# Performance work log

Hardware: AMD Instinct MI355X
Metric: run time of the kernel (lower is better)

Reference implementation:

```python
import jax, jax.numpy as jnp
import numpy as np

NUM_GRAPHS = 2048  # number of graphs in the batch (max batch id + 1)


def setup_inputs() -> dict:
    key = jax.random.key(0)
    ks = jax.random.split(key, 8)
    N, E, ND, ED, H = 100000, 400000, 256, 128, 128
    IN = ND * 3 + ED  # 896
    h = jax.random.normal(ks[0], (N, ND), dtype=jnp.float32)
    ei = jax.random.randint(ks[1], (2, E), 0, N, dtype=jnp.int64)
    ea = jax.random.normal(ks[2], (E, ED), dtype=jnp.float32)
    batch = jnp.sort(jax.random.randint(ks[3], (N,), 0, NUM_GRAPHS, dtype=jnp.int64))
    W1 = jax.random.normal(ks[4], (IN, H), dtype=jnp.float32) * (1.0 / np.sqrt(IN))
    b1 = jnp.zeros((H,), dtype=jnp.float32)
    W2 = jax.random.normal(ks[5], (H, 1), dtype=jnp.float32) * (1.0 / np.sqrt(H))
    b2 = jnp.zeros((1,), dtype=jnp.float32)
    return {"h": h, "ei": ei, "ea": ea, "batch": batch,
            "W1": W1, "b1": b1, "W2": W2, "b2": b2}


def reference(h, ei, ea, batch, W1, b1, W2, b2):
    s, t = ei[0], ei[1]
    # global_mean_pool: per-graph mean of node features
    sums = jax.ops.segment_sum(h, batch, num_segments=NUM_GRAPHS)          # [B, ND]
    counts = jax.ops.segment_sum(jnp.ones((h.shape[0],), h.dtype), batch,
                                 num_segments=NUM_GRAPHS)                   # [B]
    pooled = sums / jnp.maximum(counts, 1.0)[:, None]
    g = pooled[batch[s]]                                                    # [E, ND]
    x = jnp.concatenate([h[s], h[t], ea, g], axis=-1)                       # [E, 3*ND+ED]
    hid = jnp.maximum(x @ W1 + b1, 0.0)
    return hid @ W2 + b2                                                    # [E, 1]
```

## Files before the change

### kernel.cpp

```cpp
#include <hip/hip_runtime.h>
#include <hip/hip_bf16.h>


typedef __attribute__((ext_vector_type(8))) short bf16x8;
typedef __attribute__((ext_vector_type(4))) float f32x4;
typedef __attribute__((address_space(3))) char lds_char;
typedef __attribute__((address_space(1))) const void g_cvoid;

constexpr int kND = 256;
constexpr int kED = 128;
constexpr int kH  = 128;
constexpr int kB  = 2048;
constexpr int TM  = 128;
constexpr int kNF = 224;

__device__ __forceinline__ void gl2lds16(const void* gsrc, lds_char* ldst) {
  __builtin_amdgcn_global_load_lds((g_cvoid*)gsrc,
                                   (__attribute__((address_space(3))) void*)ldst,
                                   16, 0, 0);
}

__device__ __forceinline__ ushort f2bf(float x) {
  union { float f; unsigned u; } c; c.f = x;
  unsigned u = c.u + 0x7FFFu + ((c.u >> 16) & 1u);
  return (ushort)(u >> 16);
}
__device__ __forceinline__ float bf2f(ushort x) {
  union { unsigned u; float f; } c; c.u = ((unsigned)x) << 16;
  return c.f;
}
__device__ __forceinline__ bool data_is_f32(const void* p) {
  const unsigned* u = (const unsigned*)p;
  int cnt = 0;
  #pragma unroll
  for (int i = 0; i < 64; ++i) {
    unsigned e = (u[i] >> 7) & 0xFFu;
    cnt += (e >= 90u && e <= 140u) ? 1 : 0;
  }
  return cnt < 40;
}
__device__ __forceinline__ bool idx_is_64(const int* __restrict__ p) {
  return ((p[1] | p[3] | p[5] | p[7]) == 0) && ((p[0] | p[2] | p[4] | p[6]) != 0);
}
__device__ __forceinline__ float loadf(const void* p, int i, bool isf32) {
  return isf32 ? ((const float*)p)[i] : bf2f(((const ushort*)p)[i]);
}

__global__ __launch_bounds__(256) void pool_kernel(
    const void* __restrict__ hv, ushort* __restrict__ hbf, int preconv,
    const int* __restrict__ batch, const int* __restrict__ ei, int N,
    ushort* __restrict__ pooled) {
  const bool isf32 = data_is_f32(hv);
  const bool is64 = idx_is_64(ei);
  const int b = blockIdx.x, tid = threadIdx.x;
  __shared__ int bounds[2];
  __shared__ float sred[8][kND];
  if (tid < 2) {
    int target = b + tid;
    int lo = 0, hi = N;
    while (lo < hi) {
      int mid = (lo + hi) >> 1;
      int v = is64 ? batch[2 * mid] : batch[mid];
      if (v < target) lo = mid + 1; else hi = mid;
    }
    bounds[tid] = lo;
  }
  __syncthreads();
  const int lo = bounds[0], hi = bounds[1];
  const int dg = tid & 31;
  const int rstr = tid >> 5;
  float a[8];
  #pragma unroll
  for (int j = 0; j < 8; ++j) a[j] = 0.f;

  if (!isf32) {
    const ushort* base = (const ushort*)hv + dg * 8;
    int r = lo + rstr;
    for (; r + 8 < hi; r += 16) {
      union { uint4 v; ushort us[8]; } u0, u1;
      u0.v = *(const uint4*)(base + (size_t)r * kND);
      u1.v = *(const uint4*)(base + (size_t)(r + 8) * kND);
      #pragma unroll
      for (int j = 0; j < 8; ++j) a[j] += bf2f(u0.us[j]);
      #pragma unroll
      for (int j = 0; j < 8; ++j) a[j] += bf2f(u1.us[j]);
    }
    for (; r < hi; r += 8) {
      union { uint4 v; ushort us[8]; } u0;
      u0.v = *(const uint4*)(base + (size_t)r * kND);
      #pragma unroll
      for (int j = 0; j < 8; ++j) a[j] += bf2f(u0.us[j]);
    }
  } else if (preconv) {
    const float* base = (const float*)hv + dg * 8;
    ushort* wb = hbf + dg * 8;
    for (int r = lo + rstr; r < hi; r += 8) {
      float4 f0 = *(const float4*)(base + (size_t)r * kND);
      float4 f1 = *(const float4*)(base + (size_t)r * kND + 4);
      union { ushort us[8]; uint4 v; } cv;
      cv.us[0] = f2bf(f0.x); cv.us[1] = f2bf(f0.y);
      cv.us[2] = f2bf(f0.z); cv.us[3] = f2bf(f0.w);
      cv.us[4] = f2bf(f1.x); cv.us[5] = f2bf(f1.y);
      cv.us[6] = f2bf(f1.z); cv.us[7] = f2bf(f1.w);
      *(uint4*)(wb + (size_t)r * kND) = cv.v;
      a[0] += f0.x; a[1] += f0.y; a[2] += f0.z; a[3] += f0.w;
      a[4] += f1.x; a[5] += f1.y; a[6] += f1.z; a[7] += f1.w;
    }
  } else {
    const float* base = (const float*)hv + dg * 8;
    for (int r = lo + rstr; r < hi; r += 8) {
      float4 f0 = *(const float4*)(base + (size_t)r * kND);
      float4 f1 = *(const float4*)(base + (size_t)r * kND + 4);
      a[0] += f0.x; a[1] += f0.y; a[2] += f0.z; a[3] += f0.w;
      a[4] += f1.x; a[5] += f1.y; a[6] += f1.z; a[7] += f1.w;
    }
  }
  #pragma unroll
  for (int j = 0; j < 8; ++j) sred[rstr][dg * 8 + j] = a[j];
  __syncthreads();
  int cnt = hi - lo; if (cnt < 1) cnt = 1;
  float inv = 1.f / (float)cnt;
  float s = 0.f;
  #pragma unroll
  for (int st = 0; st < 8; ++st) s += sred[st][tid];
  pooled[(size_t)b * kND + tid] = f2bf(s * inv);
}

__global__ __launch_bounds__(256) void build_wfrag(
    const void* __restrict__ W1v, ushort* __restrict__ Wfrag) {
  const bool isf32 = data_is_f32(W1v);
  int idx = blockIdx.x * 256 + threadIdx.x;
  if (idx >= kNF * 64) return;
  int l = idx & 63, f = idx >> 6;
  int ni = f & 3, nhi = (f >> 2) & 1, ksg = f >> 3;
  int tile = ksg >> 2;
  int basek = (tile == 0) ? 512 : ((tile < 5) ? (tile - 1) * 128 : tile * 128);
  int n = nhi * 64 + ni * 16 + (l & 15);
  int k0 = basek + (ksg & 3) * 32 + (l >> 4) * 8;
  union { ushort us[8]; uint4 v; } cv;
  #pragma unroll
  for (int j = 0; j < 8; ++j)
    cv.us[j] = f2bf(loadf(W1v, (k0 + j) * kH + n, isf32));
  *(uint4*)(Wfrag + (size_t)f * 512 + l * 8) = cv.v;
}

template<bool HB, bool EA32> struct TD;
template<> struct TD<true, true> {
  static constexpr int NT = 8;
  static constexpr int ty[8]  = {0,0,1,1,2,2,3,3};
  static constexpr int sub[8] = {0,1,0,1,0,1,0,1};
  static constexpr int ksc[8] = {2,2,4,4,4,4,4,4};
  static constexpr int kg0[8] = {0,2,4,8,12,16,20,24};
  static constexpr bool tf32[8] = {1,1,0,0,0,0,0,0};
};
template<> struct TD<true, false> {
  static constexpr int NT = 7;
  static constexpr int ty[7]  = {0,1,1,2,2,3,3};
  static constexpr int sub[7] = {0,0,1,0,1,0,1};
  static constexpr int ksc[7] = {4,4,4,4,4,4,4};
  static constexpr int kg0[7] = {0,4,8,12,16,20,24};
  static constexpr bool tf32[7] = {0,0,0,0,0,0,0};
};
template<> struct TD<false, true> {
  static constexpr int NT = 12;
  static constexpr int ty[12]  = {0,0,1,1,1,1,2,2,2,2,3,3};
  static constexpr int sub[12] = {0,1,0,1,2,3,0,1,2,3,0,1};
  static constexpr int ksc[12] = {2,2,2,2,2,2,2,2,2,2,4,4};
  static constexpr int kg0[12] = {0,2,4,6,8,10,12,14,16,18,20,24};
  static constexpr bool tf32[12] = {1,1,1,1,1,1,1,1,1,1,0,0};
};
template<> struct TD<false, false> {
  static constexpr int NT = 11;
  static constexpr int ty[11]  = {0,1,1,1,1,2,2,2,2,3,3};
  static constexpr int sub[11] = {0,0,1,2,3,0,1,2,3,0,1};
  static constexpr int ksc[11] = {4,2,2,2,2,2,2,2,2,4,4};
  static constexpr int kg0[11] = {0,4,6,8,10,12,14,16,18,20,24};
  static constexpr bool tf32[11] = {0,1,1,1,1,1,1,1,1,0,0};
};

template<bool HB, bool EA32>
__device__ __forceinline__ void edge_core(
    const char* __restrict__ hsrc, const char* __restrict__ easrc,
    const ushort* __restrict__ pooled, const ushort* __restrict__ Wfrag,
    const char* XlB, lds_char* Xl3, const int* rs, const int* rt, const int* rg,
    int e0, int E, int wave, int lane, f32x4 (&acc)[4][2]) {
  using T = TD<HB, EA32>;
  const int l15 = lane & 15, quad = lane >> 4;
  const int mh = (wave & 1) * 64;
  const int nq = wave >> 1;
  const int nhi = nq >> 1;
  const int nlo = (nq & 1) * 2;
  const ushort* wl = Wfrag + (size_t)nhi * 2048 + lane * 8;
  const int cx0 = (lane & 15) * 16;
  const int rlane = lane >> 4;

  auto src_addr = [&](int t, int row) -> const char* {
    int cx = cx0 ^ ((row & 7) << 4);
    int ty = T::ty[t], sub = T::sub[t];
    if (ty == 0) {
      int e = e0 + row; if (e >= E) e = E - 1;
      return easrc + (size_t)e * (EA32 ? 512 : 256) + sub * 256 + cx;
    }
    if (ty == 1) return hsrc + (size_t)rs[row] * (HB ? 512 : 1024) + sub * 256 + cx;
    if (ty == 2) return hsrc + (size_t)rt[row] * (HB ? 512 : 1024) + sub * 256 + cx;
    return (const char*)pooled + (size_t)rg[row] * 512 + sub * 256 + cx;
  };
  auto stage = [&](int t) {
    lds_char* dst = Xl3 + (t & 1) * 32768;
    #pragma unroll
    for (int i = 0; i < 4; ++i) {
      int row = wave * 16 + i * 4 + rlane;
      gl2lds16(src_addr(t, row), dst + (wave * 16 + i * 4) * 256);
    }
  };

  stage(0);
  __syncthreads();

  #pragma unroll
  for (int t = 0; t < T::NT; ++t) {
    bf16x8 bq[8];
    #pragma unroll
    for (int ks = 0; ks < T::ksc[t]; ++ks)
      #pragma unroll
      for (int ni = 0; ni < 2; ++ni)
        bq[ks * 2 + ni] =
            *(const bf16x8*)(wl + (size_t)(T::kg0[t] + ks) * 4096 + (nlo + ni) * 512);
    __builtin_amdgcn_sched_barrier(0);
    if (t + 1 < T::NT) stage(t + 1);

    const char* xb = XlB + (t & 1) * 32768;
    #pragma unroll
    for (int ks = 0; ks < T::ksc[t]; ++ks) {
      bf16x8 af[4];
      #pragma unroll
      for (int mi = 0; mi < 4; ++mi) {
        int row = mh + mi * 16 + l15;
        int sz = (row & 7) << 4;
        const char* rb = xb + row * 256;
        if (T::tf32[t]) {
          int cb = ks * 128 + quad * 32;
          float4 f0 = *(const float4*)(rb + (cb ^ sz));
          float4 f1 = *(const float4*)(rb + ((cb + 16) ^ sz));
          union { ushort us[8]; bf16x8 v; } cv;
          cv.us[0] = f2bf(f0.x); cv.us[1] = f2bf(f0.y);
          cv.us[2] = f2bf(f0.z); cv.us[3] = f2bf(f0.w);
          cv.us[4] = f2bf(f1.x); cv.us[5] = f2bf(f1.y);
          cv.us[6] = f2bf(f1.z); cv.us[7] = f2bf(f1.w);
          af[mi] = cv.v;
        } else {
          int cb = ks * 64 + quad * 16;
          af[mi] = *(const bf16x8*)(rb + (cb ^ sz));
        }
      }
      #pragma unroll
      for (int mi = 0; mi < 4; ++mi)
        #pragma unroll
        for (int ni = 0; ni < 2; ++ni)
          acc[mi][ni] = __builtin_amdgcn_mfma_f32_16x16x32_bf16(
              af[mi], bq[ks * 2 + ni], acc[mi][ni], 0, 0, 0);
    }
    __syncthreads();
  }
}

__global__ __launch_bounds__(512, 4) void edge_kernel(
    const void* __restrict__ hv, const ushort* __restrict__ hbf, int preconv,
    const int* __restrict__ ei, const void* __restrict__ eav,
    const int* __restrict__ batch, const ushort* __restrict__ pooled,
    const ushort* __restrict__ Wfrag, const void* __restrict__ b1v,
    const void* __restrict__ W2v, const void* __restrict__ b2v,
    void* __restrict__ outv, int E) {
  __shared__ __align__(16) char XlB[2 * 32768];
  __shared__ int rs[TM], rt[TM], rg[TM];
  __shared__ float outacc[TM];
  __shared__ float b1s[kH], w2s[kH];
  lds_char* Xl3 = (lds_char*)XlB;

  const int tid = threadIdx.x;
  const int e0 = blockIdx.x * TM;
  const bool isf32 = data_is_f32(hv);
  const bool is64 = idx_is_64(ei);

  if (tid < TM) {
    int e = e0 + tid; if (e >= E) e = E - 1;
    int s = is64 ? ei[2 * e] : ei[e];
    int t = is64 ? ei[2 * (E + e)] : ei[E + e];
    rs[tid] = s;
    rt[tid] = t;
    rg[tid] = is64 ? batch[2 * s] : batch[s];
    w2s[tid] = loadf(W2v, tid, isf32);
    b1s[tid] = loadf(b1v, tid, isf32);
    outacc[tid] = 0.f;
  }
  __syncthreads();

  const int wave = tid >> 6, lane = tid & 63;
  const int l15 = lane & 15, quad = lane >> 4;
  const int mh = (wave & 1) * 64;
  const int nq = wave >> 1;
  const int nhi = nq >> 1;
  const int nlo = (nq & 1) * 2;

  f32x4 acc[4][2];
  #pragma unroll
  for (int i = 0; i < 4; ++i)
    #pragma unroll
    for (int j = 0; j < 2; ++j)
      acc[i][j] = (f32x4){0.f, 0.f, 0.f, 0.f};

  const bool hb = !isf32 || preconv;
  const char* hsrc = !isf32 ? (const char*)hv
                            : (preconv ? (const char*)hbf : (const char*)hv);
  const bool ea32 = data_is_f32(eav);

  if (hb) {
    if (ea32) edge_core<true, true >((const char*)hsrc, (const char*)eav, pooled,
                                     Wfrag, XlB, Xl3, rs, rt, rg, e0, E, wave, lane, acc);
    else      edge_core<true, false>((const char*)hsrc, (const char*)eav, pooled,
                                     Wfrag, XlB, Xl3, rs, rt, rg, e0, E, wave, lane, acc);
  } else {
    if (ea32) edge_core<false, true >((const char*)hsrc, (const char*)eav, pooled,
                                      Wfrag, XlB, Xl3, rs, rt, rg, e0, E, wave, lane, acc);
    else      edge_core<false, false>((const char*)hsrc, (const char*)eav, pooled,
                                      Wfrag, XlB, Xl3, rs, rt, rg, e0, E, wave, lane, acc);
  }

  float w2v[2], b1r[2];
  #pragma unroll
  for (int ni = 0; ni < 2; ++ni) {
    int n = nhi * 64 + (nlo + ni) * 16 + l15;
    w2v[ni] = w2s[n];
    b1r[ni] = b1s[n];
  }
  #pragma unroll
  for (int mi = 0; mi < 4; ++mi) {
    float ps[4] = {0.f, 0.f, 0.f, 0.f};
    #pragma unroll
    for (int ni = 0; ni < 2; ++ni)
      #pragma unroll
      for (int j = 0; j < 4; ++j) {
        float v = acc[mi][ni][j] + b1r[ni];
        ps[j] += (v > 0.f ? v : 0.f) * w2v[ni];
      }
    #pragma unroll
    for (int off = 1; off < 16; off <<= 1)
      #pragma unroll
      for (int j = 0; j < 4; ++j)
        ps[j] += __shfl_xor(ps[j], off, 64);
    if (l15 == 0)
      #pragma unroll
      for (int j = 0; j < 4; ++j)
        atomicAdd(&outacc[mh + mi * 16 + quad * 4 + j], ps[j]);
  }
  __syncthreads();
  if (tid < TM) {
    int e = e0 + tid;
    if (e < E) {
      float a = outacc[tid] + loadf(b2v, 0, isf32);
      if (isf32) ((float*)outv)[e] = a;
      else       ((ushort*)outv)[e] = f2bf(a);
    }
  }
}

extern "C" void kernel_launch(void* const* d_in, const int* in_sizes, int n_in,
                              void* d_out, int out_size, void* d_ws, size_t ws_size,
                              hipStream_t stream) {
  const void* h   = d_in[0];
  const int*  ei  = (const int*)d_in[1];
  const void* ea  = d_in[2];
  const int*  bat = (const int*)d_in[3];
  const void* W1  = d_in[4];
  const void* b1  = d_in[5];
  const void* W2  = d_in[6];
  const void* b2  = d_in[7];

  const int N = in_sizes[3];
  const int E = in_sizes[1] / 2;

  ushort* pooled = (ushort*)d_ws;
  ushort* Wfrag  = pooled + (size_t)kB * kND;
  ushort* hbf    = Wfrag + (size_t)kNF * 512;
  const size_t need =
      ((size_t)kB * kND + (size_t)kNF * 512 + (size_t)N * kND) * sizeof(ushort);
  const int preconv = (ws_size >= need) ? 1 : 0;

  pool_kernel<<<kB, 256, 0, stream>>>(h, hbf, preconv, bat, ei, N, pooled);
  build_wfrag<<<(kNF * 64 + 255) / 256, 256, 0, stream>>>(W1, Wfrag);
  edge_kernel<<<(E + TM - 1) / TM, 512, 0, stream>>>(
      h, hbf, preconv, ei, ea, bat, pooled, Wfrag, b1, W2, b2, d_out, E);
}
```

Baseline: 497.6 us.

## Precompute per-node and per-graph W1 projections, shrink edge GEMM to edge features

Splits the first layer by linearity. h@W1 slices are computed once per node, and pooled@W1 plus the bias once per graph; both are folded into a per-node fp32 table P12. The edge kernel then only runs an MFMA GEMM over the 128 edge-attribute columns and gathers two 128-float rows from P12 per edge before ReLU and the W2 dot. This removes the redundant per-edge GEMM over 768 gathered node and graph features, at the cost of a ~100 MB fp32 intermediate, extra launches, and scattered fp32 gathers in the edge epilogue.

```diff
diff --git a/kernel.cpp b/kernel.cpp
--- a/kernel.cpp
+++ b/kernel.cpp
@@ -124,6 +124,263 @@
   #pragma unroll
   for (int st = 0; st < 8; ++st) s += sred[st][tid];
   pooled[(size_t)b * kND + tid] = f2bf(s * inv);
+}
+
+__global__ __launch_bounds__(256) void pg_kernel(
+    const ushort* __restrict__ pooled, const void* __restrict__ W1v,
+    const void* __restrict__ b1v, float* __restrict__ Pg) {
+  const bool w32 = data_is_f32(W1v);
+  const bool b32 = data_is_f32(b1v);
+  const int tid = threadIdx.x;
+  const int g = blockIdx.x * 2 + (tid >> 7);
+  const int n = tid & 127;
+  float acc = loadf(b1v, n, b32);
+  const ushort* pr = pooled + (size_t)g * kND;
+  #pragma unroll 8
+  for (int k = 0; k < 256; ++k)
+    acc += bf2f(pr[k]) * loadf(W1v, (640 + k) * kH + n, w32);
+  Pg[(size_t)g * 128 + n] = acc;
+}
+
+__global__ __launch_bounds__(256) void build_wfrag2(
+    const void* __restrict__ W1v, ushort* __restrict__ WfragN) {
+  const bool isf32 = data_is_f32(W1v);
+  int idx = blockIdx.x * 256 + threadIdx.x;
+  if (idx >= 160 * 64) return;
+  int l = idx & 63, f = idx >> 6;
+  int row0, col;
+  int kj = (l >> 4) * 8;
+  if (f < 128) {
+    int ni = f & 3, nq = (f >> 2) & 3, ksg = f >> 4;
+    int n_l = nq * 64 + ni * 16 + (l & 15);
+    int k0 = ksg * 32 + kj;
+    row0 = (n_l < 128) ? k0 : (256 + k0);
+    col = n_l & 127;
+  } else {
+    int fe = f - 128;
+    int ni = fe & 3, nhi = (fe >> 2) & 1, ksg = fe >> 3;
+    int n = nhi * 64 + ni * 16 + (l & 15);
+    row0 = 512 + ksg * 32 + kj;
+    col = n;
+  }
+  union { ushort us[8]; uint4 v; } cv;
+  #pragma unroll
+  for (int j = 0; j < 8; ++j)
+    cv.us[j] = f2bf(loadf(W1v, (row0 + j) * kH + col, isf32));
+  *(uint4*)(WfragN + (size_t)f * 512 + l * 8) = cv.v;
+}
+
+__global__ __launch_bounds__(512, 4) void node_kernel(
+    const void* __restrict__ hv, const int* __restrict__ batch,
+    const int* __restrict__ ei, int N, const ushort* __restrict__ WfragN,
+    const float* __restrict__ Pg, float* __restrict__ P12) {
+  __shared__ __align__(16) char Xh[128 * 256];
+  __shared__ int gs[128];
+  const bool hf32 = data_is_f32(hv);
+  const bool is64 = idx_is_64(ei);
+  const int tid = threadIdx.x;
+  const int v0 = blockIdx.x * 128;
+
+  if (tid < 128) {
+    int v = v0 + tid; if (v >= N) v = N - 1;
+    gs[tid] = is64 ? batch[2 * v] : batch[v];
+  }
+
+  const int wave = tid >> 6, lane = tid & 63;
+  const int l15 = lane & 15, quad = lane >> 4;
+  const int mh = (wave & 1) * 64;
+  const int cq = wave >> 1;
+  const ushort* wl = WfragN + lane * 8;
+  const int r = tid >> 2, q = tid & 3;
+  int vr = v0 + r; if (vr >= N) vr = N - 1;
+
+  f32x4 acc[4][4];
+  #pragma unroll
+  for (int i = 0; i < 4; ++i)
+    #pragma unroll
+    for (int j = 0; j < 4; ++j)
+      acc[i][j] = (f32x4){0.f, 0.f, 0.f, 0.f};
+
+  for (int p = 0; p < 2; ++p) {
+    if (hf32) {
+      const float4* src = (const float4*)hv + (size_t)vr * 64 + p * 32 + q * 8;
+      #pragma unroll
+      for (int j = 0; j < 4; ++j) {
+        float4 f0 = src[2 * j], f1 = src[2 * j + 1];
+        union { ushort us[8]; uint4 v; } cv;
+        cv.us[0] = f2bf(f0.x); cv.us[1] = f2bf(f0.y);
+        cv.us[2] = f2bf(f0.z); cv.us[3] = f2bf(f0.w);
+        cv.us[4] = f2bf(f1.x); cv.us[5] = f2bf(f1.y);
+        cv.us[6] = f2bf(f1.z); cv.us[7] = f2bf(f1.w);
+        *(uint4*)&Xh[r * 256 + ((q * 64 + j * 16) ^ ((r & 7) << 4))] = cv.v;
+      }
+    } else {
+      const uint4* src = (const uint4*)hv + (size_t)vr * 32 + p * 16 + q * 4;
+      #pragma unroll
+      for (int j = 0; j < 4; ++j)
+        *(uint4*)&Xh[r * 256 + ((q * 64 + j * 16) ^ ((r & 7) << 4))] = src[j];
+    }
+    __syncthreads();
+    #pragma unroll
+    for (int ks = 0; ks < 4; ++ks) {
+      bf16x8 bq[4];
+      #pragma unroll
+      for (int ni = 0; ni < 4; ++ni)
+        bq[ni] = *(const bf16x8*)(wl +
+            (size_t)(((p * 4 + ks) * 16 + cq * 4 + ni)) * 512);
+      bf16x8 af[4];
+      #pragma unroll
+      for (int mi = 0; mi < 4; ++mi) {
+        int row = mh + mi * 16 + l15;
+        int cb = ks * 64 + quad * 16;
+        af[mi] = *(const bf16x8*)&Xh[row * 256 + (cb ^ ((row & 7) << 4))];
+      }
+      #pragma unroll
+      for (int mi = 0; mi < 4; ++mi)
+        #pragma unroll
+        for (int ni = 0; ni < 4; ++ni)
+          acc[mi][ni] = __builtin_amdgcn_mfma_f32_16x16x32_bf16(
+              af[mi], bq[ni], acc[mi][ni], 0, 0, 0);
+    }
+    __syncthreads();
+  }
+
+  #pragma unroll
+  for (int mi = 0; mi < 4; ++mi)
+    #pragma unroll
+    for (int ni = 0; ni < 4; ++ni) {
+      int col = cq * 64 + ni * 16 + l15;
+      #pragma unroll
+      for (int j = 0; j < 4; ++j) {
+        int row = mh + mi * 16 + quad * 4 + j;
+        int v = v0 + row;
+        if (v < N) {
+          float val = acc[mi][ni][j];
+          if (col < 128) val += Pg[(size_t)gs[row] * 128 + col];
+          P12[(size_t)v * 256 + col] = val;
+        }
+      }
+    }
+}
+
+__global__ __launch_bounds__(512, 4) void edge_kernel_new(
+    const void* __restrict__ hv, const int* __restrict__ ei,
+    const void* __restrict__ eav, const ushort* __restrict__ WfragE,
+    const float* __restrict__ P12, const void* __restrict__ W2v,
+    const void* __restrict__ b2v, void* __restrict__ outv, int E) {
+  __shared__ __align__(16) char Xe[128 * 256];
+  __shared__ int rs[TM], rt[TM];
+  __shared__ float outacc[TM];
+  __shared__ float w2s[kH];
+  const bool isf32 = data_is_f32(hv);
+  const bool ea32 = data_is_f32(eav);
+  const bool w232 = data_is_f32(W2v);
+  const bool is64 = idx_is_64(ei);
+  const int tid = threadIdx.x;
+  const int e0 = blockIdx.x * TM;
+
+  if (tid < TM) {
+    int e = e0 + tid; if (e >= E) e = E - 1;
+    rs[tid] = is64 ? ei[2 * e] : ei[e];
+    rt[tid] = is64 ? ei[2 * (E + e)] : ei[E + e];
+    w2s[tid] = loadf(W2v, tid, w232);
+    outacc[tid] = 0.f;
+  }
+
+  const int r = tid >> 2, q = tid & 3;
+  int er = e0 + r; if (er >= E) er = E - 1;
+  if (ea32) {
+    const float4* src = (const float4*)eav + (size_t)er * 32 + q * 8;
+    #pragma unroll
+    for (int j = 0; j < 4; ++j) {
+      float4 f0 = src[2 * j], f1 = src[2 * j + 1];
+      union { ushort us[8]; uint4 v; } cv;
+      cv.us[0] = f2bf(f0.x); cv.us[1] = f2bf(f0.y);
+      cv.us[2] = f2bf(f0.z); cv.us[3] = f2bf(f0.w);
+      cv.us[4] = f2bf(f1.x); cv.us[5] = f2bf(f1.y);
+      cv.us[6] = f2bf(f1.z); cv.us[7] = f2bf(f1.w);
+      *(uint4*)&Xe[r * 256 + ((q * 64 + j * 16) ^ ((r & 7) << 4))] = cv.v;
+    }
+  } else {
+    const uint4* src = (const uint4*)eav + (size_t)er * 16 + q * 4;
+    #pragma unroll
+    for (int j = 0; j < 4; ++j)
+      *(uint4*)&Xe[r * 256 + ((q * 64 + j * 16) ^ ((r & 7) << 4))] = src[j];
+  }
+  __syncthreads();
+
+  const int wave = tid >> 6, lane = tid & 63;
+  const int l15 = lane & 15, quad = lane >> 4;
+  const int mh = (wave & 1) * 64;
+  const int nq = wave >> 1;
+  const int nhi = nq >> 1;
+  const int nlo = (nq & 1) * 2;
+  const ushort* wl = WfragE + lane * 8;
+
+  f32x4 acc[4][2];
+  #pragma unroll
+  for (int i = 0; i < 4; ++i)
+    #pragma unroll
+    for (int j = 0; j < 2; ++j)
+      acc[i][j] = (f32x4){0.f, 0.f, 0.f, 0.f};
+
+  #pragma unroll
+  for (int ks = 0; ks < 4; ++ks) {
+    bf16x8 bq[2];
+    #pragma unroll
+    for (int ni = 0; ni < 2; ++ni)
+      bq[ni] = *(const bf16x8*)(wl +
+          (size_t)(ks * 8 + nhi * 4 + (nlo + ni)) * 512);
+    bf16x8 af[4];
+    #pragma unroll
+    for (int mi = 0; mi < 4; ++mi) {
+      int row = mh + mi * 16 + l15;
+      int cb = ks * 64 + quad * 16;
+      af[mi] = *(const bf16x8*)&Xe[row * 256 + (cb ^ ((row & 7) << 4))];
+    }
+    #pragma unroll
+    for (int mi = 0; mi < 4; ++mi)
+      #pragma unroll
+      for (int ni = 0; ni < 2; ++ni)
+        acc[mi][ni] = __builtin_amdgcn_mfma_f32_16x16x32_bf16(
+            af[mi], bq[ni], acc[mi][ni], 0, 0, 0);
+  }
+
+  #pragma unroll
+  for (int mi = 0; mi < 4; ++mi) {
+    float ps[4] = {0.f, 0.f, 0.f, 0.f};
+    #pragma unroll
+    for (int ni = 0; ni < 2; ++ni) {
+      int col = nhi * 64 + (nlo + ni) * 16 + l15;
+      float w2v = w2s[col];
+      #pragma unroll
+      for (int j = 0; j < 4; ++j) {
+        int row = mh + mi * 16 + quad * 4 + j;
+        float p1 = P12[(size_t)rs[row] * 256 + col];
+        float p2 = P12[(size_t)rt[row] * 256 + 128 + col];
+        float v = acc[mi][ni][j] + p1 + p2;
+        ps[j] += (v > 0.f ? v : 0.f) * w2v;
+      }
+    }
+    #pragma unroll
+    for (int off = 1; off < 16; off <<= 1)
+      #pragma unroll
+      for (int j = 0; j < 4; ++j)
+        ps[j] += __shfl_xor(ps[j], off, 64);
+    if (l15 == 0)
+      #pragma unroll
+      for (int j = 0; j < 4; ++j)
+        atomicAdd(&outacc[mh + mi * 16 + quad * 4 + j], ps[j]);
+  }
+  __syncthreads();
+  if (tid < TM) {
+    int e = e0 + tid;
+    if (e < E) {
+      float a = outacc[tid] + loadf(b2v, 0, data_is_f32(b2v));
+      if (isf32) ((float*)outv)[e] = a;
+      else       ((ushort*)outv)[e] = f2bf(a);
+    }
+  }
 }
 
 __global__ __launch_bounds__(256) void build_wfrag(
@@ -264,7 +521,7 @@
   }
 }
 
-__global__ __launch_bounds__(512, 4) void edge_kernel(
+__global__ __launch_bounds__(512, 4) void edge_kernel_old(
     const void* __restrict__ hv, const ushort* __restrict__ hbf, int preconv,
     const int* __restrict__ ei, const void* __restrict__ eav,
     const int* __restrict__ batch, const ushort* __restrict__ pooled,
@@ -380,14 +637,29 @@
   const int E = in_sizes[1] / 2;
 
   ushort* pooled = (ushort*)d_ws;
-  ushort* Wfrag  = pooled + (size_t)kB * kND;
-  ushort* hbf    = Wfrag + (size_t)kNF * 512;
-  const size_t need =
-      ((size_t)kB * kND + (size_t)kNF * 512 + (size_t)N * kND) * sizeof(ushort);
-  const int preconv = (ws_size >= need) ? 1 : 0;
-
-  pool_kernel<<<kB, 256, 0, stream>>>(h, hbf, preconv, bat, ei, N, pooled);
-  build_wfrag<<<(kNF * 64 + 255) / 256, 256, 0, stream>>>(W1, Wfrag);
-  edge_kernel<<<(E + TM - 1) / TM, 512, 0, stream>>>(
-      h, hbf, preconv, ei, ea, bat, pooled, Wfrag, b1, W2, b2, d_out, E);
-}
+  float*  Pg     = (float*)(pooled + (size_t)kB * kND);
+  ushort* WfragN = (ushort*)(Pg + (size_t)kB * 128);
+  ushort* WfragE = WfragN + (size_t)128 * 512;
+  float*  P12    = (float*)(WfragE + (size_t)32 * 512);
+  const size_t need_new = (size_t)kB * kND * 2 + (size_t)kB * 128 * 4 +
+                          (size_t)160 * 512 * 2 + (size_t)N * 256 * 4;
+
+  if (ws_size >= need_new) {
+    pool_kernel<<<kB, 256, 0, stream>>>(h, nullptr, 0, bat, ei, N, pooled);
+    build_wfrag2<<<40, 256, 0, stream>>>(W1, WfragN);
+    pg_kernel<<<kB / 2, 256, 0, stream>>>(pooled, W1, b1, Pg);
+    node_kernel<<<(N + 127) / 128, 512, 0, stream>>>(h, bat, ei, N, WfragN, Pg, P12);
+    edge_kernel_new<<<(E + TM - 1) / TM, 512, 0, stream>>>(
+        h, ei, ea, WfragE, P12, W2, b2, d_out, E);
+  } else {
+    ushort* Wfrag = pooled + (size_t)kB * kND;
+    ushort* hbf   = Wfrag + (size_t)kNF * 512;
+    const size_t need_old =
+        ((size_t)kB * kND + (size_t)kNF * 512 + (size_t)N * kND) * sizeof(ushort);
+    const int preconv = (ws_size >= need_old) ? 1 : 0;
+    pool_kernel<<<kB, 256, 0, stream>>>(h, hbf, preconv, bat, ei, N, pooled);
+    build_wfrag<<<(kNF * 64 + 255) / 256, 256, 0, stream>>>(W1, Wfrag);
+    edge_kernel_old<<<(E + TM - 1) / TM, 512, 0, stream>>>(
+        h, hbf, preconv, ei, ea, bat, pooled, Wfrag, b1, W2, b2, d_out, E);
+  }
+}
```

Measured after the change: 522.6 us. 1.05x slower.
